# Kernel optimization log

Measured on AMD Instinct MI355X. Metric: run time of the kernel, lower is better.

## Reference

```python
import jax, jax.numpy as jnp
import numpy as np

L = 2    # num_graph_layers
T = 16   # num_tasks (batch of episodes)
N = 128  # num_samples (nodes per episode)
F = 128  # num_node_feats
BN_EPS = 1e-5


def setup_inputs() -> dict:
    key = jax.random.key(0)
    ks = jax.random.split(key, 8)
    return {
        "node_feats": jax.random.normal(ks[0], (T, N, F), dtype=jnp.float32),
        "edge_feats": jax.random.uniform(ks[1], (T, N, N, F), dtype=jnp.float32),
        # Conv3d(3->1, 1x1x1) weight+bias per layer -> 3 scalars + 1 bias
        "edge_w": (jax.random.normal(ks[2], (L, 3), dtype=jnp.float32) * 0.5),
        "edge_b": (jax.random.normal(ks[3], (L,), dtype=jnp.float32) * 0.1),
        # Conv2d(2->1, 1x1, no bias) -> 2 scalars per layer
        "comb_w": (jax.random.normal(ks[4], (L, 2), dtype=jnp.float32) * 0.5),
        # Conv1d(F->F, k=1, no bias) -> [out,in] per layer
        "node_w": (jax.random.normal(ks[5], (L, F, F), dtype=jnp.float32) / np.sqrt(F).astype(np.float32)),
        # BatchNorm1d affine params
        "bn_gamma": jnp.ones((L, F), dtype=jnp.float32),
        "bn_beta": jnp.zeros((L, F), dtype=jnp.float32),
    }


def _lrelu(x):
    return jnp.where(x >= 0, x, 0.01 * x)  # torch LeakyReLU default slope


def _sim_cal(x):
    # x: [T,N,F] -> clamped [cos_sim, 1-cos_sim]: [T,2,N,N]
    g = jnp.einsum('tnf,tmf->tnm', x, x)
    nrm = jnp.linalg.norm(x, axis=-1)              # [T,N]
    denom = nrm[:, :, None] * nrm[:, None, :] + 1e-6
    sim = (g / denom)[:, None]                     # [T,1,N,N]
    pred = jnp.concatenate([sim, 1.0 - sim], axis=1)
    return jnp.clip(pred, 0.0, 1.0)


def reference(node_feats, edge_feats, edge_w, edge_b, comb_w, node_w, bn_gamma, bn_beta):
    outs = [_sim_cal(node_feats)]
    n = node_feats.shape[1]
    diag_mask = (1.0 - jnp.eye(n, dtype=node_feats.dtype))[None, :, :, None]  # [1,N,N,1]
    for l in range(L):
        x = node_feats                                     # [T,N,F]
        # --- EdgeUpdateNetwork: Conv3d(3->1,1x1x1) over channels [x_i, x_i-x_j, edge] + tanh ---
        diff = x[:, :, None, :] - x[:, None, :, :]         # [T,N,N,F]
        xi = jnp.broadcast_to(x[:, :, None, :], diff.shape)
        e = jnp.tanh(edge_w[l, 0] * xi + edge_w[l, 1] * diff
                     + edge_w[l, 2] * edge_feats + edge_b[l])
        edge_feats = e * diag_mask                         # zero diagonal
        # --- NodeUpdateNetwork ---
        aggr = edge_feats.sum(axis=2)                      # [T,N,F]
        h = _lrelu(comb_w[l, 0] * x + comb_w[l, 1] * aggr) # Conv2d(2->1) + LeakyReLU
        y = jnp.einsum('tnf,gf->tng', h, node_w[l])        # Conv1d(F->F, k=1)
        mu = y.mean(axis=(0, 1))                           # BN over (batch, length)
        var = y.var(axis=(0, 1))
        y = (y - mu) * jax.lax.rsqrt(var + BN_EPS) * bn_gamma[l] + bn_beta[l]
        node_feats = _lrelu(y)
        outs.append(_sim_cal(node_feats))
    return tuple(outs)
```

## Files before the change

### kernel.cpp

```cpp
#include <hip/hip_runtime.h>

#define T_ 16
#define N_ 128
#define F_ 128

__device__ __forceinline__ float fast_tanh(float x) {
    float e = __expf(2.0f * x);
    return 1.0f - __fdividef(2.0f, e + 1.0f);
}

__device__ __forceinline__ float lrelu(float v) {
    return v >= 0.0f ? v : 0.01f * v;
}

__global__ __launch_bounds__(128) void sim_cal_k(const float* __restrict__ x,
                                                 float* __restrict__ out) {
    __shared__ float Xs[128][132];
    __shared__ float nrm[128];
    int t = blockIdx.x, ch = blockIdx.y;
    int m = threadIdx.x;
    const float* xt = x + (size_t)t * (N_ * F_);

    int fg = (m & 31) * 4, ko = m >> 5;
    for (int kb = 0; kb < 128; kb += 4) {
        int k = kb + ko;
        float4 v = *(const float4*)(xt + k * 128 + fg);
        *(float4*)&Xs[k][fg] = v;
    }
    __syncthreads();

    float s = 0.0f;
    #pragma unroll 8
    for (int f = 0; f < 128; f += 4) {
        float4 v = *(float4*)&Xs[m][f];
        s += v.x * v.x + v.y * v.y + v.z * v.z + v.w * v.w;
    }
    nrm[m] = sqrtf(s);
    __syncthreads();

    float acc[16];
    #pragma unroll
    for (int r = 0; r < 16; ++r) acc[r] = 0.0f;

    for (int fc = 0; fc < 128; fc += 32) {
        float xm[32];
        #pragma unroll
        for (int f = 0; f < 32; f += 4) {
            float4 v = *(float4*)&Xs[m][fc + f];
            xm[f] = v.x; xm[f + 1] = v.y; xm[f + 2] = v.z; xm[f + 3] = v.w;
        }
        #pragma unroll
        for (int r = 0; r < 16; ++r) {
            int n = ch * 16 + r;
            #pragma unroll
            for (int f = 0; f < 32; f += 4) {
                float4 v = *(float4*)&Xs[n][fc + f];
                acc[r] = fmaf(xm[f], v.x,
                         fmaf(xm[f + 1], v.y,
                         fmaf(xm[f + 2], v.z,
                         fmaf(xm[f + 3], v.w, acc[r]))));
            }
        }
    }

    float nm = nrm[m];
    size_t ob = (size_t)t * 2 * 16384;
    #pragma unroll
    for (int r = 0; r < 16; ++r) {
        int n = ch * 16 + r;
        float denom = nrm[n] * nm + 1e-6f;
        float sim = __fdividef(acc[r], denom);
        float s0 = fminf(fmaxf(sim, 0.0f), 1.0f);
        float s1 = fminf(fmaxf(1.0f - sim, 0.0f), 1.0f);
        out[ob + (size_t)n * 128 + m] = s0;
        out[ob + 16384 + (size_t)n * 128 + m] = s1;
    }
}

__global__ __launch_bounds__(128) void edge_aggr_l0(const float* __restrict__ x0,
                                                    const float* __restrict__ E,
                                                    const float* __restrict__ ew,
                                                    const float* __restrict__ eb,
                                                    float* __restrict__ aggr) {
    int ti = blockIdx.x;
    int t = ti >> 7, i = ti & 127;
    int tid = threadIdx.x;
    int jl = tid >> 5, fg = tid & 31;
    float w0 = ew[0], w1 = ew[1], w2 = ew[2], b = eb[0];
    const float4* xt = (const float4*)(x0 + (size_t)t * 16384);
    const float4* Ei = (const float4*)(E + (size_t)ti * 16384);
    float4 xi = xt[i * 32 + fg];
    float ax = 0.0f, ay = 0.0f, az = 0.0f, aw = 0.0f;
    #pragma unroll 4
    for (int jb = 0; jb < 128; jb += 4) {
        int j = jb + jl;
        float4 xj = xt[j * 32 + fg];
        float4 ev = Ei[j * 32 + fg];
        if (j != i) {
            ax += fast_tanh(fmaf(w0, xi.x, fmaf(w1, xi.x - xj.x, fmaf(w2, ev.x, b))));
            ay += fast_tanh(fmaf(w0, xi.y, fmaf(w1, xi.y - xj.y, fmaf(w2, ev.y, b))));
            az += fast_tanh(fmaf(w0, xi.z, fmaf(w1, xi.z - xj.z, fmaf(w2, ev.z, b))));
            aw += fast_tanh(fmaf(w0, xi.w, fmaf(w1, xi.w - xj.w, fmaf(w2, ev.w, b))));
        }
    }
    __shared__ float4 red[128];
    red[tid] = make_float4(ax, ay, az, aw);
    __syncthreads();
    if (tid < 32) {
        float4 a = red[tid], b4 = red[tid + 32], c = red[tid + 64], d = red[tid + 96];
        float4 r;
        r.x = a.x + b4.x + c.x + d.x;
        r.y = a.y + b4.y + c.y + d.y;
        r.z = a.z + b4.z + c.z + d.z;
        r.w = a.w + b4.w + c.w + d.w;
        ((float4*)aggr)[(size_t)ti * 32 + tid] = r;
    }
}

__global__ __launch_bounds__(128) void edge_aggr_l1(const float* __restrict__ x0,
                                                    const float* __restrict__ x1,
                                                    const float* __restrict__ E,
                                                    const float* __restrict__ ew,
                                                    const float* __restrict__ eb,
                                                    float* __restrict__ aggr) {
    int ti = blockIdx.x;
    int t = ti >> 7, i = ti & 127;
    int tid = threadIdx.x;
    int jl = tid >> 5, fg = tid & 31;
    float w00 = ew[0], w01 = ew[1], w02 = ew[2], b0 = eb[0];
    float w10 = ew[3], w11 = ew[4], w12 = ew[5], b1 = eb[1];
    const float4* xt0 = (const float4*)(x0 + (size_t)t * 16384);
    const float4* xt1 = (const float4*)(x1 + (size_t)t * 16384);
    const float4* Ei = (const float4*)(E + (size_t)ti * 16384);
    float4 xi0 = xt0[i * 32 + fg];
    float4 xi1 = xt1[i * 32 + fg];
    float ax = 0.0f, ay = 0.0f, az = 0.0f, aw = 0.0f;
    #pragma unroll 2
    for (int jb = 0; jb < 128; jb += 4) {
        int j = jb + jl;
        float4 xj0 = xt0[j * 32 + fg];
        float4 xj1 = xt1[j * 32 + fg];
        float4 ev = Ei[j * 32 + fg];
        if (j != i) {
            float e0x = fast_tanh(fmaf(w00, xi0.x, fmaf(w01, xi0.x - xj0.x, fmaf(w02, ev.x, b0))));
            float e0y = fast_tanh(fmaf(w00, xi0.y, fmaf(w01, xi0.y - xj0.y, fmaf(w02, ev.y, b0))));
            float e0z = fast_tanh(fmaf(w00, xi0.z, fmaf(w01, xi0.z - xj0.z, fmaf(w02, ev.z, b0))));
            float e0w = fast_tanh(fmaf(w00, xi0.w, fmaf(w01, xi0.w - xj0.w, fmaf(w02, ev.w, b0))));
            ax += fast_tanh(fmaf(w10, xi1.x, fmaf(w11, xi1.x - xj1.x, fmaf(w12, e0x, b1))));
            ay += fast_tanh(fmaf(w10, xi1.y, fmaf(w11, xi1.y - xj1.y, fmaf(w12, e0y, b1))));
            az += fast_tanh(fmaf(w10, xi1.z, fmaf(w11, xi1.z - xj1.z, fmaf(w12, e0z, b1))));
            aw += fast_tanh(fmaf(w10, xi1.w, fmaf(w11, xi1.w - xj1.w, fmaf(w12, e0w, b1))));
        }
    }
    __shared__ float4 red[128];
    red[tid] = make_float4(ax, ay, az, aw);
    __syncthreads();
    if (tid < 32) {
        float4 a = red[tid], b4 = red[tid + 32], c = red[tid + 64], d = red[tid + 96];
        float4 r;
        r.x = a.x + b4.x + c.x + d.x;
        r.y = a.y + b4.y + c.y + d.y;
        r.z = a.z + b4.z + c.z + d.z;
        r.w = a.w + b4.w + c.w + d.w;
        ((float4*)aggr)[(size_t)ti * 32 + tid] = r;
    }
}

__global__ void transpose_w(const float* __restrict__ W, float* __restrict__ WT) {
    int l = blockIdx.y;
    int idx = blockIdx.x * 256 + threadIdx.x;
    int g = idx >> 7, f = idx & 127;
    WT[l * 16384 + f * 128 + g] = W[l * 16384 + idx];
}

__global__ void zero_bn(float* __restrict__ bn) {
    bn[threadIdx.x] = 0.0f;
}

#define ROWS 8
__global__ __launch_bounds__(128) void node_update(const float* __restrict__ x,
                                                   float* ag_y,
                                                   const float* __restrict__ cw,
                                                   const float* __restrict__ WT,
                                                   float* __restrict__ bn) {
    __shared__ float hs[ROWS][128];
    int t = blockIdx.x, ch = blockIdx.y, g = threadIdx.x;
    float c0 = cw[0], c1 = cw[1];
    size_t base = ((size_t)t * 128 + ch * ROWS) * 128;
    #pragma unroll
    for (int r = 0; r < ROWS; ++r) {
        float xv = x[base + r * 128 + g];
        float av = ag_y[base + r * 128 + g];
        hs[r][g] = lrelu(fmaf(c0, xv, c1 * av));
    }
    __syncthreads();
    float acc[ROWS];
    #pragma unroll
    for (int r = 0; r < ROWS; ++r) acc[r] = 0.0f;
    #pragma unroll 4
    for (int f2 = 0; f2 < 128; ++f2) {
        float wv = WT[f2 * 128 + g];
        #pragma unroll
        for (int r = 0; r < ROWS; ++r) acc[r] = fmaf(hs[r][f2], wv, acc[r]);
    }
    float s = 0.0f, ss = 0.0f;
    #pragma unroll
    for (int r = 0; r < ROWS; ++r) {
        ag_y[base + r * 128 + g] = acc[r];
        s += acc[r];
        ss += acc[r] * acc[r];
    }
    atomicAdd(&bn[g], s);
    atomicAdd(&bn[128 + g], ss);
}

__global__ void bn_apply(const float* __restrict__ y, const float* __restrict__ bn,
                         const float* __restrict__ gamma, const float* __restrict__ beta,
                         float* __restrict__ xout) {
    int idx = blockIdx.x * 256 + threadIdx.x;
    int g = idx & 127;
    float mu = bn[g] * (1.0f / 2048.0f);
    float var = bn[128 + g] * (1.0f / 2048.0f) - mu * mu;
    float inv = rsqrtf(var + 1e-5f);
    float v = (y[idx] - mu) * inv * gamma[g] + beta[g];
    xout[idx] = lrelu(v);
}

extern "C" void kernel_launch(void* const* d_in, const int* in_sizes, int n_in,
                              void* d_out, int out_size, void* d_ws, size_t ws_size,
                              hipStream_t stream) {
    const float* x0    = (const float*)d_in[0];
    const float* E     = (const float*)d_in[1];
    const float* ew    = (const float*)d_in[2];
    const float* eb    = (const float*)d_in[3];
    const float* cw    = (const float*)d_in[4];
    const float* nw    = (const float*)d_in[5];
    const float* gamma = (const float*)d_in[6];
    const float* beta  = (const float*)d_in[7];
    float* out = (float*)d_out;

    float* ws  = (float*)d_ws;
    float* x1  = ws;
    float* x2  = ws + 262144;
    float* yag = ws + 524288;
    float* bn  = ws + 786432;
    float* WT  = ws + 786688;

    transpose_w<<<dim3(64, 2), 256, 0, stream>>>(nw, WT);

    sim_cal_k<<<dim3(16, 8), 128, 0, stream>>>(x0, out);

    edge_aggr_l0<<<2048, 128, 0, stream>>>(x0, E, ew, eb, yag);
    zero_bn<<<1, 256, 0, stream>>>(bn);
    node_update<<<dim3(16, 16), 128, 0, stream>>>(x0, yag, cw, WT, bn);
    bn_apply<<<1024, 256, 0, stream>>>(yag, bn, gamma, beta, x1);
    sim_cal_k<<<dim3(16, 8), 128, 0, stream>>>(x1, out + 524288);

    edge_aggr_l1<<<2048, 128, 0, stream>>>(x0, x1, E, ew, eb, yag);
    zero_bn<<<1, 256, 0, stream>>>(bn);
    node_update<<<dim3(16, 16), 128, 0, stream>>>(x1, yag, cw + 2, WT + 16384, bn);
    bn_apply<<<1024, 256, 0, stream>>>(yag, bn, gamma + 128, beta + 128, x2);
    sim_cal_k<<<dim3(16, 8), 128, 0, stream>>>(x2, out + 1048576);
}
```

Before: 342.7 us.

## Fuse node update into edge aggregation and BN apply into sim kernel

Each edge-aggregation block now also computes the combine, LeakyReLU and the per-row 128x128 matvec, and accumulates the BN statistics itself, which removes the separate node_update kernel and the aggr round trip through memory. BN normalisation is folded into the similarity kernel's load stage, and the weight transpose is merged with zeroing the BN buffer. This cuts the launch count from 12 to 6. In exchange there are many more atomics per channel (one per row instead of one per 8 rows), WT is re-read by every block, and the x1 write is done only by the ch==0 blocks. Loop unroll factors also rise.

After: 411.8 us. 20.2% more time.

```diff
diff --git a/kernel.cpp b/kernel.cpp
--- a/kernel.cpp
+++ b/kernel.cpp
@@ -13,85 +13,34 @@
     return v >= 0.0f ? v : 0.01f * v;
 }
 
-__global__ __launch_bounds__(128) void sim_cal_k(const float* __restrict__ x,
-                                                 float* __restrict__ out) {
-    __shared__ float Xs[128][132];
-    __shared__ float nrm[128];
-    int t = blockIdx.x, ch = blockIdx.y;
-    int m = threadIdx.x;
-    const float* xt = x + (size_t)t * (N_ * F_);
-
-    int fg = (m & 31) * 4, ko = m >> 5;
-    for (int kb = 0; kb < 128; kb += 4) {
-        int k = kb + ko;
-        float4 v = *(const float4*)(xt + k * 128 + fg);
-        *(float4*)&Xs[k][fg] = v;
-    }
-    __syncthreads();
-
-    float s = 0.0f;
-    #pragma unroll 8
-    for (int f = 0; f < 128; f += 4) {
-        float4 v = *(float4*)&Xs[m][f];
-        s += v.x * v.x + v.y * v.y + v.z * v.z + v.w * v.w;
-    }
-    nrm[m] = sqrtf(s);
-    __syncthreads();
-
-    float acc[16];
-    #pragma unroll
-    for (int r = 0; r < 16; ++r) acc[r] = 0.0f;
-
-    for (int fc = 0; fc < 128; fc += 32) {
-        float xm[32];
-        #pragma unroll
-        for (int f = 0; f < 32; f += 4) {
-            float4 v = *(float4*)&Xs[m][fc + f];
-            xm[f] = v.x; xm[f + 1] = v.y; xm[f + 2] = v.z; xm[f + 3] = v.w;
-        }
-        #pragma unroll
-        for (int r = 0; r < 16; ++r) {
-            int n = ch * 16 + r;
-            #pragma unroll
-            for (int f = 0; f < 32; f += 4) {
-                float4 v = *(float4*)&Xs[n][fc + f];
-                acc[r] = fmaf(xm[f], v.x,
-                         fmaf(xm[f + 1], v.y,
-                         fmaf(xm[f + 2], v.z,
-                         fmaf(xm[f + 3], v.w, acc[r]))));
-            }
-        }
-    }
-
-    float nm = nrm[m];
-    size_t ob = (size_t)t * 2 * 16384;
-    #pragma unroll
-    for (int r = 0; r < 16; ++r) {
-        int n = ch * 16 + r;
-        float denom = nrm[n] * nm + 1e-6f;
-        float sim = __fdividef(acc[r], denom);
-        float s0 = fminf(fmaxf(sim, 0.0f), 1.0f);
-        float s1 = fminf(fmaxf(1.0f - sim, 0.0f), 1.0f);
-        out[ob + (size_t)n * 128 + m] = s0;
-        out[ob + 16384 + (size_t)n * 128 + m] = s1;
-    }
-}
-
-__global__ __launch_bounds__(128) void edge_aggr_l0(const float* __restrict__ x0,
-                                                    const float* __restrict__ E,
-                                                    const float* __restrict__ ew,
-                                                    const float* __restrict__ eb,
-                                                    float* __restrict__ aggr) {
+__global__ void prep_k(const float* __restrict__ W, float* __restrict__ WT,
+                       float* __restrict__ bn) {
+    int l = blockIdx.y;
+    int idx = blockIdx.x * 256 + threadIdx.x;
+    int g = idx >> 7, f = idx & 127;
+    WT[l * 16384 + f * 128 + g] = W[l * 16384 + idx];
+    if (blockIdx.x == 0) bn[l * 256 + threadIdx.x] = 0.0f;
+}
+
+__global__ __launch_bounds__(128) void edgenode_l0(const float* __restrict__ x0,
+                                                   const float* __restrict__ E,
+                                                   const float* __restrict__ ew,
+                                                   const float* __restrict__ eb,
+                                                   const float* __restrict__ cw,
+                                                   const float* __restrict__ WT,
+                                                   float* __restrict__ bn,
+                                                   float* __restrict__ ybuf) {
     int ti = blockIdx.x;
     int t = ti >> 7, i = ti & 127;
     int tid = threadIdx.x;
     int jl = tid >> 5, fg = tid & 31;
     float w0 = ew[0], w1 = ew[1], w2 = ew[2], b = eb[0];
+    float c0 = cw[0], c1 = cw[1];
     const float4* xt = (const float4*)(x0 + (size_t)t * 16384);
     const float4* Ei = (const float4*)(E + (size_t)ti * 16384);
     float4 xi = xt[i * 32 + fg];
     float ax = 0.0f, ay = 0.0f, az = 0.0f, aw = 0.0f;
-    #pragma unroll 4
+    #pragma unroll 8
     for (int jb = 0; jb < 128; jb += 4) {
         int j = jb + jl;
         float4 xj = xt[j * 32 + fg];
@@ -104,38 +53,57 @@
         }
     }
     __shared__ float4 red[128];
+    __shared__ float hs[128];
     red[tid] = make_float4(ax, ay, az, aw);
     __syncthreads();
     if (tid < 32) {
         float4 a = red[tid], b4 = red[tid + 32], c = red[tid + 64], d = red[tid + 96];
-        float4 r;
-        r.x = a.x + b4.x + c.x + d.x;
-        r.y = a.y + b4.y + c.y + d.y;
-        r.z = a.z + b4.z + c.z + d.z;
-        r.w = a.w + b4.w + c.w + d.w;
-        ((float4*)aggr)[(size_t)ti * 32 + tid] = r;
-    }
-}
-
-__global__ __launch_bounds__(128) void edge_aggr_l1(const float* __restrict__ x0,
-                                                    const float* __restrict__ x1,
-                                                    const float* __restrict__ E,
-                                                    const float* __restrict__ ew,
-                                                    const float* __restrict__ eb,
-                                                    float* __restrict__ aggr) {
+        float4 h;
+        h.x = lrelu(fmaf(c0, xi.x, c1 * (a.x + b4.x + c.x + d.x)));
+        h.y = lrelu(fmaf(c0, xi.y, c1 * (a.y + b4.y + c.y + d.y)));
+        h.z = lrelu(fmaf(c0, xi.z, c1 * (a.z + b4.z + c.z + d.z)));
+        h.w = lrelu(fmaf(c0, xi.w, c1 * (a.w + b4.w + c.w + d.w)));
+        *(float4*)&hs[tid * 4] = h;
+    }
+    __syncthreads();
+    int g = tid;
+    float acc = 0.0f;
+    #pragma unroll 4
+    for (int f = 0; f < 128; f += 4) {
+        float4 h4 = *(float4*)&hs[f];
+        acc = fmaf(h4.x, WT[f * 128 + g],
+              fmaf(h4.y, WT[(f + 1) * 128 + g],
+              fmaf(h4.z, WT[(f + 2) * 128 + g],
+              fmaf(h4.w, WT[(f + 3) * 128 + g], acc))));
+    }
+    ybuf[(size_t)ti * 128 + g] = acc;
+    atomicAdd(&bn[g], acc);
+    atomicAdd(&bn[128 + g], acc * acc);
+}
+
+__global__ __launch_bounds__(128) void edgenode_l1(const float* __restrict__ x0,
+                                                   const float* __restrict__ x1,
+                                                   const float* __restrict__ E,
+                                                   const float* __restrict__ ew,
+                                                   const float* __restrict__ eb,
+                                                   const float* __restrict__ cw,
+                                                   const float* __restrict__ WT,
+                                                   float* __restrict__ bn,
+                                                   float* __restrict__ ybuf) {
     int ti = blockIdx.x;
     int t = ti >> 7, i = ti & 127;
     int tid = threadIdx.x;
     int jl = tid >> 5, fg = tid & 31;
     float w00 = ew[0], w01 = ew[1], w02 = ew[2], b0 = eb[0];
     float w10 = ew[3], w11 = ew[4], w12 = ew[5], b1 = eb[1];
+    float c0 = cw[2], c1 = cw[3];
     const float4* xt0 = (const float4*)(x0 + (size_t)t * 16384);
     const float4* xt1 = (const float4*)(x1 + (size_t)t * 16384);
     const float4* Ei = (const float4*)(E + (size_t)ti * 16384);
     float4 xi0 = xt0[i * 32 + fg];
     float4 xi1 = xt1[i * 32 + fg];
     float ax = 0.0f, ay = 0.0f, az = 0.0f, aw = 0.0f;
-    #pragma unroll 2
+    #pragma unroll 4
     for (int jb = 0; jb < 128; jb += 4) {
         int j = jb + jl;
         float4 xj0 = xt0[j * 32 + fg];
@@ -153,77 +121,123 @@
         }
     }
     __shared__ float4 red[128];
+    __shared__ float hs[128];
     red[tid] = make_float4(ax, ay, az, aw);
     __syncthreads();
     if (tid < 32) {
         float4 a = red[tid], b4 = red[tid + 32], c = red[tid + 64], d = red[tid + 96];
-        float4 r;
-        r.x = a.x + b4.x + c.x + d.x;
-        r.y = a.y + b4.y + c.y + d.y;
-        r.z = a.z + b4.z + c.z + d.z;
-        r.w = a.w + b4.w + c.w + d.w;
-        ((float4*)aggr)[(size_t)ti * 32 + tid] = r;
-    }
-}
-
-__global__ void transpose_w(const float* __restrict__ W, float* __restrict__ WT) {
-    int l = blockIdx.y;
-    int idx = blockIdx.x * 256 + threadIdx.x;
-    int g = idx >> 7, f = idx & 127;
-    WT[l * 16384 + f * 128 + g] = W[l * 16384 + idx];
-}
-
-__global__ void zero_bn(float* __restrict__ bn) {
-    bn[threadIdx.x] = 0.0f;
-}
-
-#define ROWS 8
-__global__ __launch_bounds__(128) void node_update(const float* __restrict__ x,
-                                                   float* ag_y,
-                                                   const float* __restrict__ cw,
-                                                   const float* __restrict__ WT,
-                                                   float* __restrict__ bn) {
-    __shared__ float hs[ROWS][128];
-    int t = blockIdx.x, ch = blockIdx.y, g = threadIdx.x;
-    float c0 = cw[0], c1 = cw[1];
-    size_t base = ((size_t)t * 128 + ch * ROWS) * 128;
+        float4 h;
+        h.x = lrelu(fmaf(c0, xi1.x, c1 * (a.x + b4.x + c.x + d.x)));
+        h.y = lrelu(fmaf(c0, xi1.y, c1 * (a.y + b4.y + c.y + d.y)));
+        h.z = lrelu(fmaf(c0, xi1.z, c1 * (a.z + b4.z + c.z + d.z)));
+        h.w = lrelu(fmaf(c0, xi1.w, c1 * (a.w + b4.w + c.w + d.w)));
+        *(float4*)&hs[tid * 4] = h;
+    }
+    __syncthreads();
+    int g = tid;
+    float acc = 0.0f;
+    #pragma unroll 4
+    for (int f = 0; f < 128; f += 4) {
+        float4 h4 = *(float4*)&hs[f];
+        acc = fmaf(h4.x, WT[f * 128 + g],
+              fmaf(h4.y, WT[(f + 1) * 128 + g],
+              fmaf(h4.z, WT[(f + 2) * 128 + g],
+              fmaf(h4.w, WT[(f + 3) * 128 + g], acc))));
+    }
+    ybuf[(size_t)ti * 128 + g] = acc;
+    atomicAdd(&bn[g], acc);
+    atomicAdd(&bn[128 + g], acc * acc);
+}
+
+__global__ __launch_bounds__(128) void sim_bn_k(const float* __restrict__ y,
+                                                const float* __restrict__ bnsum,
+                                                const float* __restrict__ gamma,
+                                                const float* __restrict__ beta,
+                                                float* __restrict__ out,
+                                                float* __restrict__ xout) {
+    __shared__ float Xs[128][132];
+    __shared__ float nrm[128];
+    int t = blockIdx.x, ch = blockIdx.y;
+    int m = threadIdx.x;
+    const float* yt = y + (size_t)t * (N_ * F_);
+    int fg = (m & 31) * 4, ko = m >> 5;
+
+    bool dobn = (bnsum != nullptr);
+    float4 mu4 = make_float4(0, 0, 0, 0), inv4 = mu4, ga4 = mu4, be4 = mu4;
+    if (dobn) {
+        float4 s = *(const float4*)&bnsum[fg];
+        float4 q = *(const float4*)&bnsum[128 + fg];
+        ga4 = *(const float4*)&gamma[fg];
+        be4 = *(const float4*)&beta[fg];
+        const float r = 1.0f / 2048.0f;
+        mu4 = make_float4(s.x * r, s.y * r, s.z * r, s.w * r);
+        inv4.x = rsqrtf(q.x * r - mu4.x * mu4.x + 1e-5f);
+        inv4.y = rsqrtf(q.y * r - mu4.y * mu4.y + 1e-5f);
+        inv4.z = rsqrtf(q.z * r - mu4.z * mu4.z + 1e-5f);
+        inv4.w = rsqrtf(q.w * r - mu4.w * mu4.w + 1e-5f);
+    }
+    bool wx = (xout != nullptr) && (ch == 0);
+
+    for (int kb = 0; kb < 128; kb += 4) {
+        int k = kb + ko;
+        float4 v = *(const float4*)(yt + k * 128 + fg);
+        if (dobn) {
+            v.x = lrelu((v.x - mu4.x) * inv4.x * ga4.x + be4.x);
+            v.y = lrelu((v.y - mu4.y) * inv4.y * ga4.y + be4.y);
+            v.z = lrelu((v.z - mu4.z) * inv4.z * ga4.z + be4.z);
+            v.w = lrelu((v.w - mu4.w) * inv4.w * ga4.w + be4.w);
+        }
+        *(float4*)&Xs[k][fg] = v;
+        if (wx) *(float4*)(xout + (size_t)t * 16384 + k * 128 + fg) = v;
+    }
+    __syncthreads();
+
+    float s = 0.0f;
+    #pragma unroll 8
+    for (int f = 0; f < 128; f += 4) {
+        float4 v = *(float4*)&Xs[m][f];
+        s += v.x * v.x + v.y * v.y + v.z * v.z + v.w * v.w;
+    }
+    nrm[m] = sqrtf(s);
+    __syncthreads();
+
+    float acc[16];
     #pragma unroll
-    for (int r = 0; r < ROWS; ++r) {
-        float xv = x[base + r * 128 + g];
-        float av = ag_y[base + r * 128 + g];
-        hs[r][g] = lrelu(fmaf(c0, xv, c1 * av));
-    }
-    __syncthreads();
-    float acc[ROWS];
+    for (int r = 0; r < 16; ++r) acc[r] = 0.0f;
+
+    for (int fc = 0; fc < 128; fc += 32) {
+        float xm[32];
+        #pragma unroll
+        for (int f = 0; f < 32; f += 4) {
+            float4 v = *(float4*)&Xs[m][fc + f];
+            xm[f] = v.x; xm[f + 1] = v.y; xm[f + 2] = v.z; xm[f + 3] = v.w;
+        }
+        #pragma unroll
+        for (int r = 0; r < 16; ++r) {
+            int n = ch * 16 + r;
+            #pragma unroll
+            for (int f = 0; f < 32; f += 4) {
+                float4 v = *(float4*)&Xs[n][fc + f];
+                acc[r] = fmaf(xm[f], v.x,
+                         fmaf(xm[f + 1], v.y,
+                         fmaf(xm[f + 2], v.z,
+                         fmaf(xm[f + 3], v.w, acc[r]))));
+            }
+        }
+    }
+
+    float nm = nrm[m];
+    size_t ob = (size_t)t * 2 * 16384;
     #pragma unroll
-    for (int r = 0; r < ROWS; ++r) acc[r] = 0.0f;
-    #pragma unroll 4
-    for (int f2 = 0; f2 < 128; ++f2) {
-        float wv = WT[f2 * 128 + g];
-        #pragma unroll
-        for (int r = 0; r < ROWS; ++r) acc[r] = fmaf(hs[r][f2], wv, acc[r]);
-    }
-    float s = 0.0f, ss = 0.0f;
-    #pragma unroll
-    for (int r = 0; r < ROWS; ++r) {
-        ag_y[base + r * 128 + g] = acc[r];
-        s += acc[r];
-        ss += acc[r] * acc[r];
-    }
-    atomicAdd(&bn[g], s);
-    atomicAdd(&bn[128 + g], ss);
-}
-
-__global__ void bn_apply(const float* __restrict__ y, const float* __restrict__ bn,
-                         const float* __restrict__ gamma, const float* __restrict__ beta,
-                         float* __restrict__ xout) {
-    int idx = blockIdx.x * 256 + threadIdx.x;
-    int g = idx & 127;
-    float mu = bn[g] * (1.0f / 2048.0f);
-    float var = bn[128 + g] * (1.0f / 2048.0f) - mu * mu;
-    float inv = rsqrtf(var + 1e-5f);
-    float v = (y[idx] - mu) * inv * gamma[g] + beta[g];
-    xout[idx] = lrelu(v);
+    for (int r = 0; r < 16; ++r) {
+        int n = ch * 16 + r;
+        float denom = nrm[n] * nm + 1e-6f;
+        float sim = __fdividef(acc[r], denom);
+        float s0 = fminf(fmaxf(sim, 0.0f), 1.0f);
+        float s1 = fminf(fmaxf(1.0f - sim, 0.0f), 1.0f);
+        out[ob + (size_t)n * 128 + m] = s0;
+        out[ob + 16384 + (size_t)n * 128 + m] = s1;
+    }
 }
 
 extern "C" void kernel_launch(void* const* d_in, const int* in_sizes, int n_in,
@@ -239,26 +253,20 @@
     const float* beta  = (const float*)d_in[7];
     float* out = (float*)d_out;
 
-    float* ws  = (float*)d_ws;
-    float* x1  = ws;
-    float* x2  = ws + 262144;
-    float* yag = ws + 524288;
-    float* bn  = ws + 786432;
-    float* WT  = ws + 786688;
-
-    transpose_w<<<dim3(64, 2), 256, 0, stream>>>(nw, WT);
-
-    sim_cal_k<<<dim3(16, 8), 128, 0, stream>>>(x0, out);
-
-    edge_aggr_l0<<<2048, 128, 0, stream>>>(x0, E, ew, eb, yag);
-    zero_bn<<<1, 256, 0, stream>>>(bn);
-    node_update<<<dim3(16, 16), 128, 0, stream>>>(x0, yag, cw, WT, bn);
-    bn_apply<<<1024, 256, 0, stream>>>(yag, bn, gamma, beta, x1);
-    sim_cal_k<<<dim3(16, 8), 128, 0, stream>>>(x1, out + 524288);
-
-    edge_aggr_l1<<<2048, 128, 0, stream>>>(x0, x1, E, ew, eb, yag);
-    zero_bn<<<1, 256, 0, stream>>>(bn);
-    node_update<<<dim3(16, 16), 128, 0, stream>>>(x1, yag, cw + 2, WT + 16384, bn);
-    bn_apply<<<1024, 256, 0, stream>>>(yag, bn, gamma + 128, beta + 128, x2);
-    sim_cal_k<<<dim3(16, 8), 128, 0, stream>>>(x2, out + 1048576);
-}
+    float* ws   = (float*)d_ws;
+    float* x1   = ws;
+    float* ybuf = ws + 262144;
+    float* bn   = ws + 524288;
+    float* WT   = ws + 524800;
+
+    prep_k<<<dim3(64, 2), 256, 0, stream>>>(nw, WT, bn);
+
+    sim_bn_k<<<dim3(16, 8), 128, 0, stream>>>(x0, nullptr, nullptr, nullptr, out, nullptr);
+
+    edgenode_l0<<<2048, 128, 0, stream>>>(x0, E, ew, eb, cw, WT, bn, ybuf);
+    sim_bn_k<<<dim3(16, 8), 128, 0, stream>>>(ybuf, bn, gamma, beta, out + 524288, x1);
+
+    edgenode_l1<<<2048, 128, 0, stream>>>(x0, x1, E, ew, eb, cw, WT + 16384, bn + 256, ybuf);
+    sim_bn_k<<<dim3(16, 8), 128, 0, stream>>>(ybuf, bn + 256, gamma + 128, beta + 128,
+                                              out + 1048576, nullptr);
+}
```
